# Optimization experiments

Hardware: AMD Instinct MI355X
Metric: run time of the kernel (lower is better)

Reference implementation:

```python
import jax, jax.numpy as jnp
import numpy as np

B, S, DIN, DOUT = 4, 2048, 4096, 4096

def setup_inputs() -> dict:
    key = jax.random.key(0)
    k1, k2, k3 = jax.random.split(key, 3)
    x = jax.random.normal(k1, (B, S, DIN), dtype=jnp.float32)
    # kaiming-uniform-like scale for weight, uniform bias in [-1/sqrt(fan_in), 1/sqrt(fan_in)]
    bound_w = 1.0 / np.sqrt(DIN)
    weight = jax.random.uniform(k2, (DOUT, DIN), minval=-bound_w, maxval=bound_w, dtype=jnp.float32)
    bias = jax.random.uniform(k3, (DOUT,), minval=-bound_w, maxval=bound_w, dtype=jnp.float32)
    kk = jnp.asarray(1.0, dtype=jnp.float32)
    aa = jnp.asarray(1.0, dtype=jnp.float32)
    return {"x": x, "weight": weight, "bias": bias, "kk": kk, "aa": aa}

def reference(x, weight, bias, kk, aa):
    # Adiabatic binarization: soft-binarize weight with w_b = aa * tanh(kk * w),
    # then standard linear y = x @ w_b.T + bias. As kk -> inf, w_b -> aa*sign(w).
    w_b = aa * jnp.tanh(kk * weight)          # [DOUT, DIN]
    y = jnp.einsum('bsi,oi->bso', x, w_b)     # [B, S, DOUT]
    return y + bias
```

## Files before the change

### kernel.cpp

```cpp
#include <hip/hip_runtime.h>
#include <stdint.h>

#define B_DIM 4
#define S_DIM 2048
#define DIN   4096
#define DOUT  4096
#define M_TOT (B_DIM * S_DIM)

typedef __attribute__((ext_vector_type(8))) short  bf16x8;
typedef __attribute__((ext_vector_type(4))) float  f32x4;
typedef __attribute__((ext_vector_type(8))) unsigned short u16x8;
typedef __attribute__((ext_vector_type(4))) float  float4v;

__device__ __forceinline__ unsigned short f2b(float f) {
  union { float f; unsigned int i; } v; v.f = f;
  unsigned int r = v.i + 0x7FFFu + ((v.i >> 16) & 1u);
  return (unsigned short)(r >> 16);
}

__global__ void wb_tanh_kernel(const float4v* __restrict__ w, u16x8* __restrict__ wb,
                               const float* __restrict__ kk,
                               const float* __restrict__ aa, int n8) {
  const float k = kk[0];
  const float a = aa[0];
  int i = blockIdx.x * blockDim.x + threadIdx.x;
  const int stride = gridDim.x * blockDim.x;
  for (; i < n8; i += stride) {
    float4v v0 = w[2 * i];
    float4v v1 = w[2 * i + 1];
    u16x8 o;
#pragma unroll
    for (int j = 0; j < 4; ++j) o[j]     = f2b(a * tanhf(k * v0[j]));
#pragma unroll
    for (int j = 0; j < 4; ++j) o[j + 4] = f2b(a * tanhf(k * v1[j]));
    wb[i] = o;
  }
}

__global__ void x_cvt_kernel(const float4v* __restrict__ x, u16x8* __restrict__ xb, int n8) {
  int i = blockIdx.x * blockDim.x + threadIdx.x;
  const int stride = gridDim.x * blockDim.x;
  for (; i < n8; i += stride) {
    float4v v0 = x[2 * i];
    float4v v1 = x[2 * i + 1];
    u16x8 o;
#pragma unroll
    for (int j = 0; j < 4; ++j) o[j]     = f2b(v0[j]);
#pragma unroll
    for (int j = 0; j < 4; ++j) o[j + 4] = f2b(v1[j]);
    xb[i] = o;
  }
}

#define BM 256
#define BN 256
#define BK 64
#define NT (DIN / BK)

__device__ __forceinline__ void glds16(const unsigned short* g, unsigned short* l) {
  __builtin_amdgcn_global_load_lds(
      (const __attribute__((address_space(1))) void*)g,
      (__attribute__((address_space(3))) void*)l,
      16, 0, 0);
}

#define BARX()    __builtin_amdgcn_s_barrier()
#define LGKM0()   asm volatile("s_waitcnt lgkmcnt(0)" ::: "memory")
#define WAITVM4() asm volatile("s_waitcnt vmcnt(4)" ::: "memory")
#define WAITVM0() asm volatile("s_waitcnt vmcnt(0)" ::: "memory")

#define RD_A(dst, mi, BUFB)                                                   \
  dst[0] = *(const bf16x8*)(aRd + (BUFB) + (mi) * 2048 + blk0);               \
  dst[1] = *(const bf16x8*)(aRd + (BUFB) + (mi) * 2048 + blk1);

#define RD_B(ni, BUFB)                                                        \
  bfr[ni][0] = *(const bf16x8*)(bRd + (BUFB) + (ni) * 2048 + blk0);           \
  bfr[ni][1] = *(const bf16x8*)(bRd + (BUFB) + (ni) * 2048 + blk1);

#define MFMA_PH(AF, MB)                                                       \
  __builtin_amdgcn_s_setprio(1);                                              \
  {                                                                           \
    _Pragma("unroll")                                                         \
    for (int ks = 0; ks < 2; ++ks)                                            \
      _Pragma("unroll")                                                       \
      for (int i = 0; i < 2; ++i)                                             \
        _Pragma("unroll")                                                     \
        for (int ni = 0; ni < 4; ++ni)                                        \
          acc[(MB) + i][ni] = __builtin_amdgcn_mfma_f32_16x16x32_bf16(        \
              AF[i][ks], bfr[ni][ks], acc[(MB) + i][ni], 0, 0, 0);            \
  }                                                                           \
  __builtin_amdgcn_s_setprio(0);

#define KTILE(t, BUFB)                                                        \
  {                                                                           \
                                  \
    RD_B(0, BUFB); RD_B(1, BUFB); RD_B(2, BUFB); RD_B(3, BUFB);               \
    RD_A(afA[0], 0, BUFB); RD_A(afA[1], 1, BUFB);                             \
    issue_half(((t) + 1) * 4 + 2); issue_half(((t) + 1) * 4 + 3);             \
    BARX(); LGKM0();                                                          \
    MFMA_PH(afA, 0);                                                          \
    BARX();                                                                   \
                           \
    RD_A(afB[0], 2, BUFB); RD_A(afB[1], 3, BUFB);                             \
    RD_A(afA[0], 4, BUFB); RD_A(afA[1], 5, BUFB);                             \
    BARX(); LGKM0();                                                          \
    MFMA_PH(afB, 2);                                                          \
    BARX();                                                                   \
                                      \
    RD_A(afB[0], 6, BUFB); RD_A(afB[1], 7, BUFB);                             \
    BARX(); LGKM0();                                                          \
    MFMA_PH(afA, 4);                                                          \
    BARX();                                                                   \
       \
    issue_half(((t) + 2) * 4 + 0); issue_half(((t) + 2) * 4 + 1);             \
    BARX(); LGKM0();                                                          \
    MFMA_PH(afB, 6);                                                          \
    if ((t) + 2 < NT) { WAITVM4(); } else { WAITVM0(); }                      \
    BARX();                                                                   \
  }

__global__ __launch_bounds__(512, 2)
void gemm256_kernel(const unsigned short* __restrict__ A,
                    const unsigned short* __restrict__ Bw,
                    const float* __restrict__ bias,
                    float* __restrict__ C) {
  __shared__ unsigned short lds[2][2][BM * BK];

  const int tid  = threadIdx.x;
  const int wv   = tid >> 6;
  const int lane = tid & 63;
  const int l15  = lane & 15;
  const int quad = lane >> 4;
  const int l7   = lane & 7;
  const int rlan = lane >> 3;

  const int swz = ((blockIdx.x & 7) << 6) | (blockIdx.x >> 3);
  const int bm  = (swz & 31) << 8;
  const int bn  = (swz >> 5) << 8;

  const unsigned short* aLane = A  + (size_t)(bm + wv * 16 + rlan) * DIN + ((l7 ^ rlan) << 3);
  const unsigned short* bLane = Bw + (size_t)(bn + wv * 16 + rlan) * DIN + ((l7 ^ rlan) << 3);

  auto issue_half = [&](int idx) {
    const int kt = idx >> 2;
    if (kt >= NT) return;
    const int hh  = idx & 3;
    const int mat = hh >> 1;
    const int hr  = hh & 1;
    const unsigned short* g =
        (mat ? bLane : aLane) + (size_t)hr * (128 * DIN) + (size_t)kt * BK;
    unsigned short* l = &lds[kt & 1][mat][hr * (128 * BK) + wv * (16 * BK)];
    glds16(g, l);
    glds16(g + 8 * DIN, l + 8 * BK);
  };

  issue_half(0); issue_half(1); issue_half(2); issue_half(3);
  issue_half(4); issue_half(5);

  const int hA   = wv >> 2;
  const int hB   = (wv & 3) >> 1;
  const int wloc = wv & 1;
  const char* aRd = (const char*)&lds[0][0][0] + hA * 16384 + l15 * 128;
  const char* bRd = (const char*)&lds[0][1][0] + hB * 16384 + wloc * 8192 + l15 * 128;
  const int blk0 = ((0 + quad) ^ l7) * 16;
  const int blk1 = ((4 + quad) ^ l7) * 16;

  f32x4  acc[8][4] = {};
  bf16x8 bfr[4][2], afA[2][2], afB[2][2];

  WAITVM4();
  BARX();

#pragma unroll 1
  for (int t = 0; t < NT; t += 2) {
    KTILE(t, 0);
    KTILE(t + 1, 65536);
  }

  const int wm = (wv >> 2) * 128;
  const int wn = (wv & 3) * 64;
#pragma unroll
  for (int ni = 0; ni < 4; ++ni) {
    const int col = bn + wn + ni * 16 + l15;
    const float bv = bias[col];
#pragma unroll
    for (int mi = 0; mi < 8; ++mi) {
      const int row0 = bm + wm + mi * 16 + quad * 4;
#pragma unroll
      for (int e = 0; e < 4; ++e)
        C[(size_t)(row0 + e) * DOUT + col] = acc[mi][ni][e] + bv;
    }
  }
}

extern "C" void kernel_launch(void* const* d_in, const int* in_sizes, int n_in,
                              void* d_out, int out_size, void* d_ws, size_t ws_size,
                              hipStream_t stream) {
  const float* x    = (const float*)d_in[0];
  const float* w    = (const float*)d_in[1];
  const float* bias = (const float*)d_in[2];
  const float* kk   = (const float*)d_in[3];
  const float* aa   = (const float*)d_in[4];
  float* out = (float*)d_out;

  unsigned short* wb = (unsigned short*)d_ws;
  unsigned short* xb = wb + (size_t)DOUT * DIN;

  wb_tanh_kernel<<<2048, 256, 0, stream>>>(
      (const float4v*)w, (u16x8*)wb, kk, aa, DOUT * DIN / 8);
  x_cvt_kernel<<<4096, 256, 0, stream>>>(
      (const float4v*)x, (u16x8*)xb, M_TOT * DIN / 8);

  gemm256_kernel<<<dim3(512), dim3(512), 0, stream>>>(xb, wb, bias, out);
}
```

Measured before the change: 532.5 us.

## Fuse conversion kernels and restructure GEMM k-loop schedule and tile mapping

Merges the weight-tanh and x-conversion kernels into one launch that splits work by block index, removing one kernel launch and its tail. Inside the GEMM, the k-tile schedule changes: each phase now works on one k-half across four A fragments, using a partial lgkmcnt wait before the barrier. Each k-tile's global-to-LDS loads are issued in one batch instead of two split halves, and the block-to-tile mapping is changed so each XCD covers a contiguous 8x8 group of tiles for better L2 reuse. This risks register pressure from the extra fragment buffers and less overlap between loads and MFMA.

```diff
diff --git a/kernel.cpp b/kernel.cpp
--- a/kernel.cpp
+++ b/kernel.cpp
@@ -18,37 +18,39 @@
   return (unsigned short)(r >> 16);
 }
 
-__global__ void wb_tanh_kernel(const float4v* __restrict__ w, u16x8* __restrict__ wb,
-                               const float* __restrict__ kk,
-                               const float* __restrict__ aa, int n8) {
-  const float k = kk[0];
-  const float a = aa[0];
-  int i = blockIdx.x * blockDim.x + threadIdx.x;
-  const int stride = gridDim.x * blockDim.x;
-  for (; i < n8; i += stride) {
-    float4v v0 = w[2 * i];
-    float4v v1 = w[2 * i + 1];
-    u16x8 o;
-#pragma unroll
-    for (int j = 0; j < 4; ++j) o[j]     = f2b(a * tanhf(k * v0[j]));
-#pragma unroll
-    for (int j = 0; j < 4; ++j) o[j + 4] = f2b(a * tanhf(k * v1[j]));
-    wb[i] = o;
-  }
-}
-
-__global__ void x_cvt_kernel(const float4v* __restrict__ x, u16x8* __restrict__ xb, int n8) {
-  int i = blockIdx.x * blockDim.x + threadIdx.x;
-  const int stride = gridDim.x * blockDim.x;
-  for (; i < n8; i += stride) {
-    float4v v0 = x[2 * i];
-    float4v v1 = x[2 * i + 1];
-    u16x8 o;
-#pragma unroll
-    for (int j = 0; j < 4; ++j) o[j]     = f2b(v0[j]);
-#pragma unroll
-    for (int j = 0; j < 4; ++j) o[j + 4] = f2b(v1[j]);
-    xb[i] = o;
+__global__ void cvt_fused_kernel(const float4v* __restrict__ w, u16x8* __restrict__ wbo,
+                                 const float4v* __restrict__ x, u16x8* __restrict__ xbo,
+                                 const float* __restrict__ kk,
+                                 const float* __restrict__ aa) {
+  const int bid = blockIdx.x;
+  if (bid < 2048) {
+    const float k = kk[0];
+    const float a = aa[0];
+    const int n8 = DOUT * DIN / 8;
+    int i = bid * 256 + threadIdx.x;
+    for (; i < n8; i += 2048 * 256) {
+      float4v v0 = w[2 * i];
+      float4v v1 = w[2 * i + 1];
+      u16x8 o;
+#pragma unroll
+      for (int j = 0; j < 4; ++j) o[j]     = f2b(a * tanhf(k * v0[j]));
+#pragma unroll
+      for (int j = 0; j < 4; ++j) o[j + 4] = f2b(a * tanhf(k * v1[j]));
+      wbo[i] = o;
+    }
+  } else {
+    const int n8 = M_TOT * DIN / 8;
+    int i = (bid - 2048) * 256 + threadIdx.x;
+    for (; i < n8; i += 4096 * 256) {
+      float4v v0 = x[2 * i];
+      float4v v1 = x[2 * i + 1];
+      u16x8 o;
+#pragma unroll
+      for (int j = 0; j < 4; ++j) o[j]     = f2b(v0[j]);
+#pragma unroll
+      for (int j = 0; j < 4; ++j) o[j + 4] = f2b(v1[j]);
+      xbo[i] = o;
+    }
   }
 }
 
@@ -66,56 +68,59 @@
 
 #define BARX()    __builtin_amdgcn_s_barrier()
 #define LGKM0()   asm volatile("s_waitcnt lgkmcnt(0)" ::: "memory")
-#define WAITVM4() asm volatile("s_waitcnt vmcnt(4)" ::: "memory")
+#define LGKM4()   asm volatile("s_waitcnt lgkmcnt(4)" ::: "memory")
+#define WAITVM8() asm volatile("s_waitcnt vmcnt(8)" ::: "memory")
 #define WAITVM0() asm volatile("s_waitcnt vmcnt(0)" ::: "memory")
 
-#define RD_A(dst, mi, BUFB)                                                   \
-  dst[0] = *(const bf16x8*)(aRd + (BUFB) + (mi) * 2048 + blk0);               \
-  dst[1] = *(const bf16x8*)(aRd + (BUFB) + (mi) * 2048 + blk1);
-
-#define RD_B(ni, BUFB)                                                        \
-  bfr[ni][0] = *(const bf16x8*)(bRd + (BUFB) + (ni) * 2048 + blk0);           \
-  bfr[ni][1] = *(const bf16x8*)(bRd + (BUFB) + (ni) * 2048 + blk1);
-
-#define MFMA_PH(AF, MB)                                                       \
+#define RDB(dst, BLK, BUFB)                                                   \
+  dst[0] = *(const bf16x8*)(bRd + (BUFB) + 0 * 2048 + (BLK));                 \
+  dst[1] = *(const bf16x8*)(bRd + (BUFB) + 1 * 2048 + (BLK));                 \
+  dst[2] = *(const bf16x8*)(bRd + (BUFB) + 2 * 2048 + (BLK));                 \
+  dst[3] = *(const bf16x8*)(bRd + (BUFB) + 3 * 2048 + (BLK));
+
+#define RDA4(dst, MB, BLK, BUFB)                                              \
+  dst[0] = *(const bf16x8*)(aRd + (BUFB) + ((MB) + 0) * 2048 + (BLK));        \
+  dst[1] = *(const bf16x8*)(aRd + (BUFB) + ((MB) + 1) * 2048 + (BLK));        \
+  dst[2] = *(const bf16x8*)(aRd + (BUFB) + ((MB) + 2) * 2048 + (BLK));        \
+  dst[3] = *(const bf16x8*)(aRd + (BUFB) + ((MB) + 3) * 2048 + (BLK));
+
+#define MFMA_PH(AF, BF, MB)                                                   \
   __builtin_amdgcn_s_setprio(1);                                              \
   {                                                                           \
     _Pragma("unroll")                                                         \
-    for (int ks = 0; ks < 2; ++ks)                                            \
+    for (int i = 0; i < 4; ++i)                                               \
       _Pragma("unroll")                                                       \
-      for (int i = 0; i < 2; ++i)                                             \
-        _Pragma("unroll")                                                     \
-        for (int ni = 0; ni < 4; ++ni)                                        \
-          acc[(MB) + i][ni] = __builtin_amdgcn_mfma_f32_16x16x32_bf16(        \
-              AF[i][ks], bfr[ni][ks], acc[(MB) + i][ni], 0, 0, 0);            \
+      for (int ni = 0; ni < 4; ++ni)                                          \
+        acc[(MB) + i][ni] = __builtin_amdgcn_mfma_f32_16x16x32_bf16(          \
+            AF[i], BF[ni], acc[(MB) + i][ni], 0, 0, 0);                       \
   }                                                                           \
   __builtin_amdgcn_s_setprio(0);
 
 #define KTILE(t, BUFB)                                                        \
   {                                                                           \
-                                  \
-    RD_B(0, BUFB); RD_B(1, BUFB); RD_B(2, BUFB); RD_B(3, BUFB);               \
-    RD_A(afA[0], 0, BUFB); RD_A(afA[1], 1, BUFB);                             \
-    issue_half(((t) + 1) * 4 + 2); issue_half(((t) + 1) * 4 + 3);             \
-    BARX(); LGKM0();                                                          \
-    MFMA_PH(afA, 0);                                                          \
-    BARX();                                                                   \
-                           \
-    RD_A(afB[0], 2, BUFB); RD_A(afB[1], 3, BUFB);                             \
-    RD_A(afA[0], 4, BUFB); RD_A(afA[1], 5, BUFB);                             \
-    BARX(); LGKM0();                                                          \
-    MFMA_PH(afB, 2);                                                          \
-    BARX();                                                                   \
-                                      \
-    RD_A(afB[0], 6, BUFB); RD_A(afB[1], 7, BUFB);                             \
-    BARX(); LGKM0();                                                          \
-    MFMA_PH(afA, 4);                                                          \
+                                         \
+    RDB(bfr0, blk0, BUFB);                                                    \
+    RDA4(afA, 0, blk0, BUFB);                                                 \
+    LGKM4(); BARX(); LGKM0();                                                 \
+    MFMA_PH(afA, bfr0, 0);                                                    \
+    BARX();                                                                   \
+                                         \
+    RDA4(afB, 4, blk0, BUFB);                                                 \
+    RDB(bfr1, blk1, BUFB);                                                    \
+    LGKM4(); BARX(); LGKM0();                                                 \
+    MFMA_PH(afB, bfr0, 4);                                                    \
+    BARX();                                                                   \
+                         \
+    RDA4(afA, 0, blk1, BUFB);                                                 \
+    RDA4(afB, 4, blk1, BUFB);                                                 \
+    LGKM4(); BARX(); LGKM0();                                                 \
+    MFMA_PH(afA, bfr1, 0);                                                    \
     BARX();                                                                   \
        \
-    issue_half(((t) + 2) * 4 + 0); issue_half(((t) + 2) * 4 + 1);             \
-    BARX(); LGKM0();                                                          \
-    MFMA_PH(afB, 6);                                                          \
-    if ((t) + 2 < NT) { WAITVM4(); } else { WAITVM0(); }                      \
+    stage((t) + 2);                                                           \
+    BARX();                                                                   \
+    MFMA_PH(afB, bfr1, 4);                                                    \
+    if ((t) + 2 < NT) { WAITVM8(); } else { WAITVM0(); }                      \
     BARX();                                                                   \
   }
 
@@ -134,28 +139,32 @@
   const int l7   = lane & 7;
   const int rlan = lane >> 3;
 
-  const int swz = ((blockIdx.x & 7) << 6) | (blockIdx.x >> 3);
-  const int bm  = (swz & 31) << 8;
-  const int bn  = (swz >> 5) << 8;
+  const int xcd = blockIdx.x & 7;
+  const int idx = blockIdx.x >> 3;
+  const int bm  = ((((xcd & 3) << 3) | (idx & 7)) << 8);
+  const int bn  = ((((xcd >> 2) << 3) | (idx >> 3)) << 8);
 
   const unsigned short* aLane = A  + (size_t)(bm + wv * 16 + rlan) * DIN + ((l7 ^ rlan) << 3);
   const unsigned short* bLane = Bw + (size_t)(bn + wv * 16 + rlan) * DIN + ((l7 ^ rlan) << 3);
 
-  auto issue_half = [&](int idx) {
-    const int kt = idx >> 2;
+  auto stage = [&](int kt) {
     if (kt >= NT) return;
-    const int hh  = idx & 3;
-    const int mat = hh >> 1;
-    const int hr  = hh & 1;
-    const unsigned short* g =
-        (mat ? bLane : aLane) + (size_t)hr * (128 * DIN) + (size_t)kt * BK;
-    unsigned short* l = &lds[kt & 1][mat][hr * (128 * BK) + wv * (16 * BK)];
-    glds16(g, l);
-    glds16(g + 8 * DIN, l + 8 * BK);
+    const int buf = kt & 1;
+    const size_t ko = (size_t)kt * BK;
+#pragma unroll
+    for (int hr = 0; hr < 2; ++hr) {
+      const unsigned short* ga = aLane + (size_t)hr * (128 * DIN) + ko;
+      unsigned short* la = &lds[buf][0][hr * (128 * BK) + wv * (16 * BK)];
+      glds16(ga, la);
+      glds16(ga + 8 * DIN, la + 8 * BK);
+      const unsigned short* gb = bLane + (size_t)hr * (128 * DIN) + ko;
+      unsigned short* lb = &lds[buf][1][hr * (128 * BK) + wv * (16 * BK)];
+      glds16(gb, lb);
+      glds16(gb + 8 * DIN, lb + 8 * BK);
+    }
   };
 
-  issue_half(0); issue_half(1); issue_half(2); issue_half(3);
-  issue_half(4); issue_half(5);
+  stage(0); stage(1);
 
   const int hA   = wv >> 2;
   const int hB   = (wv & 3) >> 1;
@@ -166,9 +175,9 @@
   const int blk1 = ((4 + quad) ^ l7) * 16;
 
   f32x4  acc[8][4] = {};
-  bf16x8 bfr[4][2], afA[2][2], afB[2][2];
-
-  WAITVM4();
+  bf16x8 bfr0[4], bfr1[4], afA[4], afB[4];
+
+  WAITVM8();
   BARX();
 
 #pragma unroll 1
@@ -206,10 +215,8 @@
   unsigned short* wb = (unsigned short*)d_ws;
   unsigned short* xb = wb + (size_t)DOUT * DIN;
 
-  wb_tanh_kernel<<<2048, 256, 0, stream>>>(
-      (const float4v*)w, (u16x8*)wb, kk, aa, DOUT * DIN / 8);
-  x_cvt_kernel<<<4096, 256, 0, stream>>>(
-      (const float4v*)x, (u16x8*)xb, M_TOT * DIN / 8);
+  cvt_fused_kernel<<<6144, 256, 0, stream>>>(
+      (const float4v*)w, (u16x8*)wb, (const float4v*)x, (u16x8*)xb, kk, aa);
 
   gemm256_kernel<<<dim3(512), dim3(512), 0, stream>>>(xb, wb, bias, out);
 }
```

Measured after the change: 524.0 us. Within noise of the previous version (-1.6%).
